# Kernel tuning notes

Measured on AMD Instinct MI355X. Metric: run time of the kernel, lower is better.

## Reference

```python
import jax, jax.numpy as jnp
import numpy as np

H = 1024
W = 1024
FID = 100          # palette_fidelity
NF = 8             # number of IFS functions in the FunctionSet stub
N_POINTS = 1 << 20
K_STEPS = 20


def setup_inputs() -> dict:
    key = jax.random.key(0)
    ks = jax.random.split(key, 8)
    # xy ~ Normal(0, initial_sigma=2.0), c ~ Uniform(0,1)
    xy = 2.0 * jax.random.normal(ks[0], (N_POINTS, 2), dtype=jnp.float32)
    c = jax.random.uniform(ks[1], (N_POINTS, 1), dtype=jnp.float32)
    points = jnp.concatenate([xy, c], axis=1)                      # [N,3]
    # per-step random function selection (external FunctionSet randomness)
    choices = jax.random.randint(ks[2], (K_STEPS, N_POINTS), 0, NF, dtype=jnp.int32)
    # contractive-ish affine maps
    A = 0.5 * jax.random.normal(ks[3], (NF, 2, 2), dtype=jnp.float32)
    b = jax.random.normal(ks[4], (NF, 2), dtype=jnp.float32)
    func_colors = jax.random.uniform(ks[5], (NF,), dtype=jnp.float32)
    palette = jax.random.uniform(ks[6], (FID + 1, 4), dtype=jnp.float32)
    # view window [-3,3]x[-3,3] -> min_vec / range_vec exactly as in __init__
    x_min, x_max, y_min, y_max = -3.0, 3.0, -3.0, 3.0
    min_vec = jnp.array([x_min, y_min], dtype=jnp.float32)
    range_vec = jnp.array([W / (x_max - x_min), H / (y_max - y_min)], dtype=jnp.float32)
    raw_image0 = jnp.zeros((4, H, W), dtype=jnp.float32)
    return dict(points=points, choices=choices, A=A, b=b,
                func_colors=func_colors, palette=palette,
                min_vec=min_vec, range_vec=range_vec,
                raw_image0=raw_image0, skip_first_k=2)


def reference(points, choices, A, b, func_colors, palette,
              min_vec, range_vec, raw_image0, skip_first_k):
    def step(carry, inputs):
        pts, img = carry
        k, idx = inputs                                   # idx: [N] function ids
        xy, c = pts[:, :2], pts[:, 2]
        # FunctionSet: per-point affine map + color blend (flame IFS)
        new_xy = jnp.einsum('nij,nj->ni', A[idx], xy) + b[idx]
        new_c = 0.5 * (c + func_colors[idx])
        pts = jnp.concatenate([new_xy, new_c[:, None]], axis=1)
        # palette interpolation (matches floor/ceil lerp in the original)
        _c = new_c * FID
        cf = jnp.floor(_c)
        cc = jnp.ceil(_c)
        t = (_c - cf)[:, None]
        cfi = jnp.clip(cf, 0, FID).astype(jnp.int32)
        cci = jnp.clip(cc, 0, FID).astype(jnp.int32)
        color_vectors = t * palette[cci] + (1.0 - t) * palette[cfi]   # [N,4]
        # bin indices: ((xy - min) * range).long()  (truncation toward zero)
        bins = ((new_xy - min_vec) * range_vec).astype(jnp.int32)
        xb, yb = bins[:, 0], bins[:, 1]
        ok = (xb >= 0) & (xb < W) & (yb >= 0) & (yb < H) & (k >= skip_first_k)
        xb = jnp.where(ok, xb, 0)
        yb = jnp.where(ok, yb, 0)
        vals = jnp.where(ok[:, None], color_vectors, 0.0)             # [N,4]
        # original indexes raw_image[color][x_bins, y_bins]
        img = img.at[:, xb, yb].add(vals.T)
        return (pts, img), None

    k_steps = choices.shape[0]
    (_, img), _ = jax.lax.scan(step, (points, raw_image0),
                               (jnp.arange(k_steps), choices))
    return img
```

## Files before the change

kernel.cpp:

```cpp
#include <hip/hip_runtime.h>

constexpr int H = 1024, W = 1024, FID = 100, NF = 8;
constexpr int NPTS = 1 << 20, KSTEPS = 20;
constexpr int HW = H * W;

constexpr int NTX = 16, NTY = 32, NTILES = NTX * NTY;
constexpr int TPIX = 64 * 32;
constexpr int NBLK = 2048;
constexpr int PPB = NPTS / NBLK;
constexpr int PPT = PPB / 256;
constexpr int NBLK_C = 1024;
constexpr int SEG_N = NTILES * NBLK;
constexpr int CHUNK = 16384;
constexpr int TH    = 4096;
constexpr int MAXREC = NPTS * KSTEPS;
constexpr int K4_GRID = MAXREC / CHUNK;
constexpr int K4_BS  = 512;
constexpr int MAXVIS = K4_GRID + NTILES;
constexpr unsigned INV = 0xFFFFFFFFu;
constexpr float QSCALE = 16384.0f;
constexpr float QINV   = 1.0f / 16384.0f;
constexpr float FXS  = 131072.0f;
constexpr float FXSI = 1.0f / 131072.0f;

__device__ __forceinline__ void decode_rec(unsigned r, const float4* sPal,
                                           int& pix, float& v0, float& v1,
                                           float& v2, float& v3) {
    pix = (int)(r & 2047u);
    const float _c = (float)(r >> 11) * QINV;
    const float cf = floorf(_c);
    const float tt = _c - cf;
    const int cfi = (int)fminf(fmaxf(cf, 0.f), (float)FID);
    const int cci = (int)fminf(fmaxf(ceilf(_c), 0.f), (float)FID);
    const float4 pc = sPal[cci];
    const float4 pf = sPal[cfi];
    const float omt = 1.f - tt;
    v0 = tt * pc.x + omt * pf.x;
    v1 = tt * pc.y + omt * pf.y;
    v2 = tt * pc.z + omt * pf.z;
    v3 = tt * pc.w + omt * pf.w;
}

__device__ __forceinline__ unsigned long long pack2(float a, float b) {
    const unsigned ua = __float2uint_rn(a * FXS);
    const unsigned ub = __float2uint_rn(b * FXS);
    return (unsigned long long)ua | ((unsigned long long)ub << 32);
}

__global__ __launch_bounds__(256)
void count_kernel(const float* __restrict__ points,
                  const int* __restrict__ choices,
                  const float* __restrict__ A,
                  const float* __restrict__ b,
                  const float* __restrict__ minv,
                  const float* __restrict__ rangev,
                  const int* __restrict__ skipp,
                  unsigned* __restrict__ hist,
                  unsigned long long* __restrict__ packed)
{
    __shared__ float sA[NF * 4], sB[NF * 2];
    __shared__ unsigned shist[4][NTILES];
    const int t = threadIdx.x;
    if (t < NF * 4) sA[t] = A[t];
    if (t < NF * 2) sB[t] = b[t];
    for (int i = t; i < 4 * NTILES; i += 256) ((unsigned*)shist)[i] = 0u;
    __syncthreads();

    const int blk = blockIdx.x;
    const int base = blk * 1024;
    const int n0 = base + 4 * t;
    const float mx = minv[0], my = minv[1], rx = rangev[0], ry = rangev[1];
    const int skip = skipp[0];
    const int wv = t >> 6;

    const float4 f0 = *(const float4*)&points[3 * n0 + 0];
    const float4 f1 = *(const float4*)&points[3 * n0 + 4];
    const float4 f2 = *(const float4*)&points[3 * n0 + 8];
    float px_[4] = { f0.x, f0.w, f1.z, f2.y };
    float py_[4] = { f0.y, f1.x, f1.w, f2.z };

    unsigned long long pk_[4] = { 0ull, 0ull, 0ull, 0ull };
    unsigned ctile_[4] = { INV, INV, INV, INV };
    unsigned ccnt_[4]  = { 0u, 0u, 0u, 0u };

#pragma unroll
    for (int k = 0; k < KSTEPS; ++k) {
        const int4 cv = *(const int4*)&choices[k * NPTS + n0];
        const int idxs[4] = { cv.x & 7, cv.y & 7, cv.z & 7, cv.w & 7 };
#pragma unroll
        for (int j = 0; j < 4; ++j) {
            const int idx = idxs[j];
            pk_[j] |= (unsigned long long)idx << (3 * k);
            const float nx = sA[idx*4+0]*px_[j] + sA[idx*4+1]*py_[j] + sB[idx*2+0];
            const float ny = sA[idx*4+2]*px_[j] + sA[idx*4+3]*py_[j] + sB[idx*2+1];
            px_[j] = nx; py_[j] = ny;
            const int xb = (int)((nx - mx) * rx);
            const int yb = (int)((ny - my) * ry);
            if (k >= skip && (unsigned)xb < (unsigned)W && (unsigned)yb < (unsigned)H) {
                const unsigned tile = (unsigned)(((xb >> 6) << 5) | (yb >> 5));
                if (tile == ctile_[j]) { ++ccnt_[j]; }
                else {
                    if (ctile_[j] != INV) atomicAdd(&shist[wv][ctile_[j]], ccnt_[j]);
                    ctile_[j] = tile; ccnt_[j] = 1;
                }
            }
        }
    }
#pragma unroll
    for (int j = 0; j < 4; ++j) {
        if (ctile_[j] != INV) atomicAdd(&shist[wv][ctile_[j]], ccnt_[j]);
        packed[n0 + j] = pk_[j];
    }
    __syncthreads();
    for (int tt = t; tt < NTILES; tt += 256) {
        hist[tt * NBLK + 2 * blk]     = shist[0][tt] + shist[1][tt];
        hist[tt * NBLK + 2 * blk + 1] = shist[2][tt] + shist[3][tt];
    }
}

__global__ __launch_bounds__(1024)
void scan1_kernel(unsigned* __restrict__ hist, unsigned* __restrict__ sums)
{
    __shared__ unsigned buf[2][1024];
    const int t = threadIdx.x;
    const int base = blockIdx.x * NBLK;
    const unsigned v0 = hist[base + 2 * t];
    const unsigned v1 = hist[base + 2 * t + 1];
    int src = 0;
    buf[0][t] = v0 + v1; __syncthreads();
    for (int off = 1; off < 1024; off <<= 1) {
        unsigned val = buf[src][t];
        if (t >= off) val += buf[src][t - off];
        buf[1 - src][t] = val; src ^= 1; __syncthreads();
    }
    const unsigned incl = buf[src][t];
    const unsigned ex = incl - (v0 + v1);
    hist[base + 2 * t]     = ex;
    hist[base + 2 * t + 1] = ex + v0;
    if (t == 1023) sums[blockIdx.x] = incl;
}

__global__ __launch_bounds__(512)
void scan2v_kernel(unsigned* __restrict__ sums,
                   unsigned* __restrict__ dstart,
                   unsigned* __restrict__ vstart)
{
    __shared__ unsigned buf[2][512];
    const int t = threadIdx.x;
    const unsigned len = sums[t];

    int src = 0;
    buf[0][t] = len; __syncthreads();
    for (int off = 1; off < 512; off <<= 1) {
        unsigned val = buf[src][t];
        if (t >= off) val += buf[src][t - off];
        buf[1 - src][t] = val; src ^= 1; __syncthreads();
    }
    unsigned incl = buf[src][t];
    sums[t] = incl - len;
    if (t == 511) sums[512] = incl;

    const unsigned dlen = (len >= (unsigned)TH) ? len : 0u;
    __syncthreads();
    buf[0][t] = dlen; src = 0; __syncthreads();
    for (int off = 1; off < 512; off <<= 1) {
        unsigned val = buf[src][t];
        if (t >= off) val += buf[src][t - off];
        buf[1 - src][t] = val; src ^= 1; __syncthreads();
    }
    unsigned dincl = buf[src][t];
    const unsigned dexcl = dincl - dlen;
    dstart[t] = dexcl;
    if (t == 511) dstart[512] = dincl;

    unsigned c = 0;
    if (dlen) c = (dexcl + dlen - 1) / CHUNK - dexcl / CHUNK + 1;
    __syncthreads();
    buf[0][t] = c; src = 0; __syncthreads();
    for (int off = 1; off < 512; off <<= 1) {
        unsigned val = buf[src][t];
        if (t >= off) val += buf[src][t - off];
        buf[1 - src][t] = val; src ^= 1; __syncthreads();
    }
    unsigned vincl = buf[src][t];
    vstart[t] = vincl - c;
    if (t == 511) vstart[512] = vincl;
}

__global__ __launch_bounds__(256)
void scatter_kernel(const float* __restrict__ points,
                    const unsigned long long* __restrict__ packed,
                    const float* __restrict__ A,
                    const float* __restrict__ b,
                    const float* __restrict__ fc,
                    const float* __restrict__ minv,
                    const float* __restrict__ rangev,
                    const int* __restrict__ skipp,
                    const unsigned* __restrict__ scanb,
                    const unsigned* __restrict__ sums,
                    unsigned* __restrict__ records)
{
    __shared__ float sA[NF * 4], sB[NF * 2], sFC[NF];
    __shared__ unsigned sCur[NTILES];

    const int t = threadIdx.x;
    const int blk = blockIdx.x;
    if (t < NF * 4) sA[t] = A[t];
    if (t < NF * 2) sB[t] = b[t];
    if (t < NF)     sFC[t] = fc[t];
    for (int tt = t; tt < NTILES; tt += 256)
        sCur[tt] = scanb[tt * NBLK + blk] + sums[tt];
    __syncthreads();

    const int base = blk * PPB;
    const float mx = minv[0], my = minv[1], rx = rangev[0], ry = rangev[1];
    const int skip = skipp[0];

    for (int p = 0; p < PPT; ++p) {
        const int n = base + p * 256 + t;
        float x = points[3*n], y = points[3*n+1], c = points[3*n+2];
        const unsigned long long pk = packed[n];

#pragma unroll
        for (int k = 0; k < KSTEPS; ++k) {
            const int idx = (int)((pk >> (3 * k)) & 7ull);
            const float nx = sA[idx*4+0]*x + sA[idx*4+1]*y + sB[idx*2+0];
            const float ny = sA[idx*4+2]*x + sA[idx*4+3]*y + sB[idx*2+1];
            c = 0.5f * (c + sFC[idx]);
            x = nx; y = ny;
            const int xb = (int)((nx - mx) * rx);
            const int yb = (int)((ny - my) * ry);
            if (k >= skip && (unsigned)xb < (unsigned)W && (unsigned)yb < (unsigned)H) {
                const unsigned tile = (unsigned)(((xb >> 6) << 5) | (yb >> 5));
                const unsigned q = (unsigned)__float2int_rn(c * (100.0f * QSCALE));
                const unsigned rec = (q << 11) | (unsigned)(((xb & 63) << 5) | (yb & 31));
                const unsigned pos = atomicAdd(&sCur[tile], 1u);
                records[pos] = rec;
            }
        }
    }
}

__global__ __launch_bounds__(K4_BS)
void accum_slot_kernel(const unsigned* __restrict__ records,
                       const unsigned* __restrict__ sums,
                       const unsigned* __restrict__ dstart,
                       const unsigned* __restrict__ vstart,
                       const float* __restrict__ palette,
                       float* __restrict__ slots)
{
    __shared__ unsigned long long img01[TPIX];
    __shared__ unsigned long long img23[TPIX];
    __shared__ float4 sPal[FID + 1];
    __shared__ unsigned tstart[NTILES + 1];
    __shared__ unsigned dst[NTILES + 1];
    __shared__ unsigned vst[NTILES];
    const int t = threadIdx.x;
    for (int i = t; i < NTILES + 1; i += K4_BS) { tstart[i] = sums[i]; dst[i] = dstart[i]; }
    for (int i = t; i < NTILES; i += K4_BS) vst[i] = vstart[i];
    for (int i = t; i < (FID + 1) * 4; i += K4_BS) ((float*)sPal)[i] = palette[i];
    __syncthreads();

    const unsigned dtotal = dst[NTILES];
    const unsigned r0 = (unsigned)blockIdx.x * CHUNK;
    if (r0 >= dtotal) return;
    const unsigned r1 = min(r0 + (unsigned)CHUNK, dtotal);

    int lo = 0, hi = NTILES;
    while (lo < hi) {
        const int mid = (lo + hi + 1) >> 1;
        if (dst[mid] <= r0) lo = mid; else hi = mid - 1;
    }

    for (int tile = lo; tile < NTILES && dst[tile] < r1; ++tile) {
        const unsigned sd = max(dst[tile], r0);
        const unsigned ed = min(dst[tile + 1], r1);
        if (sd >= ed) continue;
        const unsigned gs = tstart[tile] + (sd - dst[tile]);
        const unsigned ge = gs + (ed - sd);

        for (int i = t; i < TPIX; i += K4_BS) { img01[i] = 0ull; img23[i] = 0ull; }
        __syncthreads();

        for (unsigned i = gs + t; i < ge; i += K4_BS) {
            int pix; float v0, v1, v2, v3;
            decode_rec(records[i], sPal, pix, v0, v1, v2, v3);
            atomicAdd(&img01[pix], pack2(v0, v1));
            atomicAdd(&img23[pix], pack2(v2, v3));
        }
        __syncthreads();

        const unsigned slot = vst[tile] + ((unsigned)blockIdx.x - dst[tile] / CHUNK);
        float* sp = slots + (size_t)slot * (4 * TPIX);
        for (int i2 = t; i2 < TPIX; i2 += K4_BS) {
            const unsigned long long a = img01[i2];
            const unsigned long long bb = img23[i2];
            sp[0 * TPIX + i2] = (float)(unsigned)(a  & 0xFFFFFFFFu) * FXSI;
            sp[1 * TPIX + i2] = (float)(unsigned)(a  >> 32)         * FXSI;
            sp[2 * TPIX + i2] = (float)(unsigned)(bb & 0xFFFFFFFFu) * FXSI;
            sp[3 * TPIX + i2] = (float)(unsigned)(bb >> 32)         * FXSI;
        }
        __syncthreads();
    }
}

__global__ __launch_bounds__(256)
void reduce_kernel(const float* __restrict__ slots,
                   const unsigned* __restrict__ vstart,
                   const unsigned* __restrict__ sums,
                   const unsigned* __restrict__ records,
                   const float* __restrict__ palette,
                   const float* __restrict__ raw0,
                   float* __restrict__ out)
{
    __shared__ unsigned long long l01[256];
    __shared__ unsigned long long l23[256];
    __shared__ float4 sPal[FID + 1];
    const int T = blockIdx.x >> 3;
    const int g = blockIdx.x & 7;
    const int t = threadIdx.x;
    for (int i = t; i < (FID + 1) * 4; i += 256) ((float*)sPal)[i] = palette[i];
    l01[t] = 0ull; l23[t] = 0ull;
    __syncthreads();

    const unsigned v0 = vstart[T], v1 = vstart[T + 1];
    const unsigned s = sums[T], e = sums[T + 1];
    const int ch = t >> 6;
    const int f4 = ch * (TPIX / 4) + (g * 256 >> 2) + (t & 63);

    float4 acc = {0.f, 0.f, 0.f, 0.f};
    for (unsigned v = v0; v < v1; ++v) {
        const float4 sv = ((const float4*)(slots + (size_t)v * (4 * TPIX)))[f4];
        acc.x += sv.x; acc.y += sv.y; acc.z += sv.z; acc.w += sv.w;
    }

    if (v0 == v1 && e > s) {
        for (unsigned i = s + t; i < e; i += 256) {
            const unsigned r = records[i];
            const int pix = (int)(r & 2047u);
            if ((pix >> 8) == g) {
                int dummy; float w0, w1, w2, w3;
                decode_rec(r, sPal, dummy, w0, w1, w2, w3);
                const int lp = pix & 255;
                atomicAdd(&l01[lp], pack2(w0, w1));
                atomicAdd(&l23[lp], pack2(w2, w3));
            }
        }
    }
    __syncthreads();

    const int lbase = (t & 63) * 4;
#pragma unroll
    for (int j = 0; j < 4; ++j) {
        const int lp = lbase + j;
        float v;
        if (ch == 0)      v = (float)(unsigned)(l01[lp] & 0xFFFFFFFFu) * FXSI;
        else if (ch == 1) v = (float)(unsigned)(l01[lp] >> 32) * FXSI;
        else if (ch == 2) v = (float)(unsigned)(l23[lp] & 0xFFFFFFFFu) * FXSI;
        else              v = (float)(unsigned)(l23[lp] >> 32) * FXSI;
        if (j == 0) acc.x += v;
        else if (j == 1) acc.y += v;
        else if (j == 2) acc.z += v;
        else acc.w += v;
    }

    const int lpix = g * 256 + lbase;
    const int px = lpix >> 5, py = lpix & 31;
    const int tx = T >> 5, ty = T & 31;
    const size_t o = (size_t)ch * HW + (size_t)(tx * 64 + px) * W + (ty * 32 + py);
    const float4 r = *(const float4*)(raw0 + o);
    acc.x += r.x; acc.y += r.y; acc.z += r.z; acc.w += r.w;
    *(float4*)(out + o) = acc;
}

__global__ __launch_bounds__(256)
void flame_kernel_planar(const float* __restrict__ points,
                         const int* __restrict__ choices,
                         const float* __restrict__ A,
                         const float* __restrict__ b,
                         const float* __restrict__ fc,
                         const float* __restrict__ palette,
                         const float* __restrict__ min_vec,
                         const float* __restrict__ range_vec,
                         const int* __restrict__ skipp,
                         float* __restrict__ out)
{
    __shared__ float sA[NF * 4];
    __shared__ float sB[NF * 2];
    __shared__ float sFC[NF];
    __shared__ float4 sPal[FID + 1];
    const int t = threadIdx.x;
    if (t < NF * 4) sA[t] = A[t];
    if (t < NF * 2) sB[t] = b[t];
    if (t < NF)     sFC[t] = fc[t];
    for (int i = t; i < (FID + 1) * 4; i += 256) ((float*)sPal)[i] = palette[i];
    __syncthreads();

    const int n = blockIdx.x * 256 + t;
    float x = points[3 * n], y = points[3 * n + 1], c = points[3 * n + 2];
    const float mx = min_vec[0], my = min_vec[1];
    const float rx = range_vec[0], ry = range_vec[1];
    const int skip = skipp[0];

    for (int k = 0; k < KSTEPS; ++k) {
        const int idx = choices[k * NPTS + n];
        const float nx = sA[idx*4+0]*x + sA[idx*4+1]*y + sB[idx*2+0];
        const float ny = sA[idx*4+2]*x + sA[idx*4+3]*y + sB[idx*2+1];
        c = 0.5f * (c + sFC[idx]);
        x = nx; y = ny;
        const float _c = c * (float)FID;
        const float cf = floorf(_c);
        const float tt = _c - cf;
        const int cfi = (int)fminf(fmaxf(cf, 0.f), (float)FID);
        const int cci = (int)fminf(fmaxf(ceilf(_c), 0.f), (float)FID);
        const float4 pc = sPal[cci];
        const float4 pf = sPal[cfi];
        const int xb = (int)((nx - mx) * rx);
        const int yb = (int)((ny - my) * ry);
        if (k >= skip && (unsigned)xb < (unsigned)W && (unsigned)yb < (unsigned)H) {
            const int p = xb * W + yb;
            const float omt = 1.f - tt;
            atomicAdd(out + p + 0 * HW, tt * pc.x + omt * pf.x);
            atomicAdd(out + p + 1 * HW, tt * pc.y + omt * pf.y);
            atomicAdd(out + p + 2 * HW, tt * pc.z + omt * pf.z);
            atomicAdd(out + p + 3 * HW, tt * pc.w + omt * pf.w);
        }
    }
}

extern "C" void kernel_launch(void* const* d_in, const int* in_sizes, int n_in,
                              void* d_out, int out_size, void* d_ws, size_t ws_size,
                              hipStream_t stream) {
    const float* points    = (const float*)d_in[0];
    const int*   choices   = (const int*)d_in[1];
    const float* A         = (const float*)d_in[2];
    const float* b         = (const float*)d_in[3];
    const float* fc        = (const float*)d_in[4];
    const float* palette   = (const float*)d_in[5];
    const float* min_vec   = (const float*)d_in[6];
    const float* range_vec = (const float*)d_in[7];
    const float* raw0      = (const float*)d_in[8];
    const int*   skipp     = (const int*)d_in[9];
    float* out = (float*)d_out;
    const size_t img_bytes = (size_t)4 * HW * sizeof(float);

    const size_t rec_off  = 0;
    const size_t rec_cap  = (size_t)MAXREC * 4;
    const size_t sums_off = rec_off + rec_cap;
    const size_t dst_off  = sums_off + 4096;
    const size_t vst_off  = dst_off + 4096;
    const size_t slot_off = vst_off + 4096;
    const size_t slot_cap = (size_t)MAXVIS * (4 * TPIX) * sizeof(float);
    const size_t pk_off   = slot_off;
    const size_t hist_off = slot_off + (size_t)NPTS * 8;
    const size_t need1    = slot_off + slot_cap;

    unsigned* sums = (unsigned*)((char*)d_ws + sums_off);
    unsigned* recs = (unsigned*)((char*)d_ws + rec_off);

    if (ws_size >= need1) {
        unsigned* hist   = (unsigned*)((char*)d_ws + hist_off);
        unsigned* dstart = (unsigned*)((char*)d_ws + dst_off);
        unsigned* vstart = (unsigned*)((char*)d_ws + vst_off);
        float*    slots  = (float*)((char*)d_ws + slot_off);
        unsigned long long* packed = (unsigned long long*)((char*)d_ws + pk_off);

        count_kernel<<<NBLK_C, 256, 0, stream>>>(
            points, choices, A, b, min_vec, range_vec, skipp, hist, packed);
        scan1_kernel<<<NTILES, 1024, 0, stream>>>(hist, sums);
        scan2v_kernel<<<1, 512, 0, stream>>>(sums, dstart, vstart);
        scatter_kernel<<<NBLK, 256, 0, stream>>>(
            points, packed, A, b, fc, min_vec, range_vec, skipp, hist, sums, recs);
        accum_slot_kernel<<<K4_GRID, K4_BS, 0, stream>>>(
            recs, sums, dstart, vstart, palette, slots);
        reduce_kernel<<<NTILES * 8, 256, 0, stream>>>(
            slots, vstart, sums, recs, palette, raw0, out);
    } else {
        hipMemcpyAsync(out, raw0, img_bytes, hipMemcpyDeviceToDevice, stream);
        flame_kernel_planar<<<NPTS / 256, 256, 0, stream>>>(
            points, choices, A, b, fc, palette, min_vec, range_vec, skipp, out);
    }
}
```

Before: 311.4 us.

## Vectorize record loads, raise sparse threshold, use one block per tile in reduce

The accumulation kernel now reads records four at a time with uint4 loads and masks out entries outside the tile's range. The reduce kernel switches from eight 256-thread blocks per tile to one 1024-thread block per tile. That block holds the full tile's shared histogram, so sparse tiles decode each record once instead of having all eight sub-blocks scan and filter it. TH is raised, which shifts more tiles onto the sparse shared-memory path. The costs are 32KB of shared memory per reduce block, fewer and larger blocks, and a risk of misaligned uint4 reads at the edges of the records buffer.

```diff
diff --git a/kernel.cpp b/kernel.cpp
--- a/kernel.cpp
+++ b/kernel.cpp
@@ -12,7 +12,7 @@
 constexpr int NBLK_C = 1024;
 constexpr int SEG_N = NTILES * NBLK;
 constexpr int CHUNK = 16384;
-constexpr int TH    = 4096;
+constexpr int TH    = 16384;
 constexpr int MAXREC = NPTS * KSTEPS;
 constexpr int K4_GRID = MAXREC / CHUNK;
 constexpr int K4_BS  = 512;
@@ -282,11 +282,20 @@
         for (int i = t; i < TPIX; i += K4_BS) { img01[i] = 0ull; img23[i] = 0ull; }
         __syncthreads();
 
-        for (unsigned i = gs + t; i < ge; i += K4_BS) {
-            int pix; float v0, v1, v2, v3;
-            decode_rec(records[i], sPal, pix, v0, v1, v2, v3);
-            atomicAdd(&img01[pix], pack2(v0, v1));
-            atomicAdd(&img23[pix], pack2(v2, v3));
+        const unsigned abase = gs & ~3u;
+        for (unsigned i = abase + 4u * (unsigned)t; i < ge; i += 4u * K4_BS) {
+            const uint4 r4 = *(const uint4*)&records[i];
+            const unsigned rr[4] = { r4.x, r4.y, r4.z, r4.w };
+#pragma unroll
+            for (int j = 0; j < 4; ++j) {
+                const unsigned ri = i + (unsigned)j;
+                if (ri >= gs && ri < ge) {
+                    int pix; float v0, v1, v2, v3;
+                    decode_rec(rr[j], sPal, pix, v0, v1, v2, v3);
+                    atomicAdd(&img01[pix], pack2(v0, v1));
+                    atomicAdd(&img23[pix], pack2(v2, v3));
+                }
+            }
         }
         __syncthreads();
 
@@ -304,7 +313,7 @@
     }
 }
 
-__global__ __launch_bounds__(256)
+__global__ __launch_bounds__(1024)
 void reduce_kernel(const float* __restrict__ slots,
                    const unsigned* __restrict__ vstart,
                    const unsigned* __restrict__ sums,
@@ -313,64 +322,67 @@
                    const float* __restrict__ raw0,
                    float* __restrict__ out)
 {
-    __shared__ unsigned long long l01[256];
-    __shared__ unsigned long long l23[256];
+    __shared__ unsigned long long l01[TPIX];
+    __shared__ unsigned long long l23[TPIX];
     __shared__ float4 sPal[FID + 1];
-    const int T = blockIdx.x >> 3;
-    const int g = blockIdx.x & 7;
-    const int t = threadIdx.x;
-    for (int i = t; i < (FID + 1) * 4; i += 256) ((float*)sPal)[i] = palette[i];
-    l01[t] = 0ull; l23[t] = 0ull;
-    __syncthreads();
+    const int T = blockIdx.x;
+    const int t = threadIdx.x;
+    for (int i = t; i < (FID + 1) * 4; i += 1024) ((float*)sPal)[i] = palette[i];
 
     const unsigned v0 = vstart[T], v1 = vstart[T + 1];
     const unsigned s = sums[T], e = sums[T + 1];
-    const int ch = t >> 6;
-    const int f4 = ch * (TPIX / 4) + (g * 256 >> 2) + (t & 63);
-
-    float4 acc = {0.f, 0.f, 0.f, 0.f};
+    const bool sparse = (v0 == v1) && (e > s);
+    if (sparse) for (int i = t; i < TPIX; i += 1024) { l01[i] = 0ull; l23[i] = 0ull; }
+    __syncthreads();
+
+    float4 acc0 = {0.f,0.f,0.f,0.f}, acc1 = {0.f,0.f,0.f,0.f};
     for (unsigned v = v0; v < v1; ++v) {
-        const float4 sv = ((const float4*)(slots + (size_t)v * (4 * TPIX)))[f4];
-        acc.x += sv.x; acc.y += sv.y; acc.z += sv.z; acc.w += sv.w;
-    }
-
-    if (v0 == v1 && e > s) {
-        for (unsigned i = s + t; i < e; i += 256) {
-            const unsigned r = records[i];
-            const int pix = (int)(r & 2047u);
-            if ((pix >> 8) == g) {
-                int dummy; float w0, w1, w2, w3;
-                decode_rec(r, sPal, dummy, w0, w1, w2, w3);
-                const int lp = pix & 255;
-                atomicAdd(&l01[lp], pack2(w0, w1));
-                atomicAdd(&l23[lp], pack2(w2, w3));
+        const float4* sp = (const float4*)(slots + (size_t)v * (4 * TPIX));
+        const float4 a = sp[t];
+        const float4 bq = sp[t + 1024];
+        acc0.x += a.x;  acc0.y += a.y;  acc0.z += a.z;  acc0.w += a.w;
+        acc1.x += bq.x; acc1.y += bq.y; acc1.z += bq.z; acc1.w += bq.w;
+    }
+
+    if (sparse) {
+        for (unsigned i = s + t; i < e; i += 1024) {
+            int pix; float w0, w1, w2, w3;
+            decode_rec(records[i], sPal, pix, w0, w1, w2, w3);
+            atomicAdd(&l01[pix], pack2(w0, w1));
+            atomicAdd(&l23[pix], pack2(w2, w3));
+        }
+    }
+    __syncthreads();
+
+    const int tx = T >> 5, ty = T & 31;
+#pragma unroll
+    for (int half = 0; half < 2; ++half) {
+        const int f  = t + half * 1024;
+        const int ch = f >> 9;
+        const int q  = f & 511;
+        const int p0 = q * 4;
+        float4 acc = half ? acc1 : acc0;
+        if (sparse) {
+#pragma unroll
+            for (int j = 0; j < 4; ++j) {
+                const int p = p0 + j;
+                float vadd;
+                if (ch == 0)      vadd = (float)(unsigned)(l01[p] & 0xFFFFFFFFu) * FXSI;
+                else if (ch == 1) vadd = (float)(unsigned)(l01[p] >> 32) * FXSI;
+                else if (ch == 2) vadd = (float)(unsigned)(l23[p] & 0xFFFFFFFFu) * FXSI;
+                else              vadd = (float)(unsigned)(l23[p] >> 32) * FXSI;
+                if (j == 0) acc.x += vadd;
+                else if (j == 1) acc.y += vadd;
+                else if (j == 2) acc.z += vadd;
+                else acc.w += vadd;
             }
         }
-    }
-    __syncthreads();
-
-    const int lbase = (t & 63) * 4;
-#pragma unroll
-    for (int j = 0; j < 4; ++j) {
-        const int lp = lbase + j;
-        float v;
-        if (ch == 0)      v = (float)(unsigned)(l01[lp] & 0xFFFFFFFFu) * FXSI;
-        else if (ch == 1) v = (float)(unsigned)(l01[lp] >> 32) * FXSI;
-        else if (ch == 2) v = (float)(unsigned)(l23[lp] & 0xFFFFFFFFu) * FXSI;
-        else              v = (float)(unsigned)(l23[lp] >> 32) * FXSI;
-        if (j == 0) acc.x += v;
-        else if (j == 1) acc.y += v;
-        else if (j == 2) acc.z += v;
-        else acc.w += v;
-    }
-
-    const int lpix = g * 256 + lbase;
-    const int px = lpix >> 5, py = lpix & 31;
-    const int tx = T >> 5, ty = T & 31;
-    const size_t o = (size_t)ch * HW + (size_t)(tx * 64 + px) * W + (ty * 32 + py);
-    const float4 r = *(const float4*)(raw0 + o);
-    acc.x += r.x; acc.y += r.y; acc.z += r.z; acc.w += r.w;
-    *(float4*)(out + o) = acc;
+        const int px = p0 >> 5, py = p0 & 31;
+        const size_t o = (size_t)ch * HW + (size_t)(tx * 64 + px) * W + (ty * 32 + py);
+        const float4 r = *(const float4*)(raw0 + o);
+        acc.x += r.x; acc.y += r.y; acc.z += r.z; acc.w += r.w;
+        *(float4*)(out + o) = acc;
+    }
 }
 
 __global__ __launch_bounds__(256)
@@ -473,7 +485,7 @@
             points, packed, A, b, fc, min_vec, range_vec, skipp, hist, sums, recs);
         accum_slot_kernel<<<K4_GRID, K4_BS, 0, stream>>>(
             recs, sums, dstart, vstart, palette, slots);
-        reduce_kernel<<<NTILES * 8, 256, 0, stream>>>(
+        reduce_kernel<<<NTILES, 1024, 0, stream>>>(
             slots, vstart, sums, recs, palette, raw0, out);
     } else {
         hipMemcpyAsync(out, raw0, img_bytes, hipMemcpyDeviceToDevice, stream);
```

Result: no change. 307.5 us (-1.2%).
